# Optimization experiments

Measured on AMD Instinct MI355X. Metric: run time of the kernel, lower is better.

## Reference

```python
import jax, jax.numpy as jnp
import numpy as np

T = 16384       # video length (frames)
C = 7           # out_features = d_model = num surgical phases
F_DIM = 2048    # mstcn_f_dim (spatial feature dim)
LEN_Q = 30      # sliding window length
N_HEADS = 4
D_K = 64        # attn_dim = min(64, mstcn_f_maps=64)
D_FF = 64       # d_ff = mstcn_f_maps


def setup_inputs() -> dict:
    key = jax.random.key(0)
    ks = jax.random.split(key, 10)
    w = lambda i, shape: jax.random.normal(ks[i], shape, jnp.float32) * 0.05
    return {
        "x": jax.random.normal(ks[0], (1, C, T), jnp.float32),
        "long_feature": jax.random.normal(ks[1], (1, T, F_DIM), jnp.float32),
        "W_fc": w(2, (C, F_DIM)),              # nn.Linear(mstcn_f_dim, out_features, bias=False)
        "W_q": w(3, (N_HEADS * D_K, C)),
        "W_k": w(4, (N_HEADS * D_K, C)),
        "W_v": w(5, (N_HEADS * D_K, C)),
        "W_o": w(6, (C, N_HEADS * D_K)),
        "ln1_g": jnp.ones((C,), jnp.float32),
        "ln1_b": jnp.zeros((C,), jnp.float32),
        "W_ff1": w(7, (D_FF, C)),
        "W_ff2": w(8, (C, D_FF)),
        "ln2_g": jnp.ones((C,), jnp.float32),
        "ln2_b": jnp.zeros((C,), jnp.float32),
    }


def layer_norm(x, g, b, eps=1e-5):
    mu = x.mean(-1, keepdims=True)
    var = ((x - mu) ** 2).mean(-1, keepdims=True)
    return (x - mu) * jax.lax.rsqrt(var + eps) * g + b


def reference(x, long_feature, W_fc, W_q, W_k, W_v, W_o, ln1_g, ln1_b, W_ff1, W_ff2, ln2_g, ln2_b):
    # --- vectorized sliding-window (replaces the Python loop of zeros/cat/stack) ---
    feats = x[0].T                                            # (T, C)
    padded = jnp.concatenate([jnp.zeros((LEN_Q - 1, C), feats.dtype), feats], axis=0)
    idx = jnp.arange(T)[:, None] + jnp.arange(LEN_Q)[None, :]  # window ends at frame i
    inputs = padded[idx]                                       # (T, LEN_Q, C)

    # --- spatial embedding: feas = tanh(fc(long_feature)).transpose(0,1) ---
    feas = jnp.tanh(long_feature[0] @ W_fc.T)[:, None, :]      # (T, 1, C)

    # --- decoder layer: cross MHA(query=feas, kv=inputs) + residual + LN ---
    q = (feas @ W_q.T).reshape(T, 1, N_HEADS, D_K).transpose(0, 2, 1, 3)       # (T,H,1,Dk)
    k = (inputs @ W_k.T).reshape(T, LEN_Q, N_HEADS, D_K).transpose(0, 2, 1, 3)  # (T,H,Lq,Dk)
    v = (inputs @ W_v.T).reshape(T, LEN_Q, N_HEADS, D_K).transpose(0, 2, 1, 3)  # (T,H,Lq,Dk)
    scores = jnp.einsum('thqd,thkd->thqk', q, k) / np.float32(np.sqrt(D_K))
    attn = jax.nn.softmax(scores, axis=-1)
    ctx = jnp.einsum('thqk,thkd->thqd', attn, v)
    ctx = ctx.transpose(0, 2, 1, 3).reshape(T, 1, N_HEADS * D_K)
    out = layer_norm(ctx @ W_o.T + feas, ln1_g, ln1_b)         # (T, 1, C)

    # --- position-wise FFN + residual + LN ---
    ff = jax.nn.relu(out @ W_ff1.T) @ W_ff2.T
    out = layer_norm(ff + out, ln2_g, ln2_b)
    return out[:, 0]                                           # (T, C) per-frame logits
```

## Files before the change

kernel.cpp:

```cpp
#include <hip/hip_runtime.h>
#include <math.h>

#define T_FRAMES 16384
#define FDIM 2048
#define LQ 30
#define FPB 16

__global__ __launch_bounds__(448) void setup_kernel(
    const float* __restrict__ Wq, const float* __restrict__ Wk,
    const float* __restrict__ Wv, const float* __restrict__ Wo,
    float* __restrict__ AM) {
  const int e = threadIdx.x;
  if (e >= 392) return;
  const int which = e / 196;
  const int r = e % 196;
  const int h = r / 49;
  const int rr = r % 49;
  const int c = rr / 7;
  const int c2 = rr % 7;
  float s = 0.0f;
  if (which == 0) {
    for (int d = 0; d < 64; ++d)
      s = fmaf(Wq[(h * 64 + d) * 7 + c], Wk[(h * 64 + d) * 7 + c2], s);
  } else {
    for (int d = 0; d < 64; ++d)
      s = fmaf(Wo[c * 256 + h * 64 + d], Wv[(h * 64 + d) * 7 + c2], s);
  }
  AM[e] = s;
}

__global__ __launch_bounds__(256) void fused_kernel(
    const float* __restrict__ lf,
    const float* __restrict__ Wfc,
    const float* __restrict__ x,
    const float* __restrict__ AM,
    const float* __restrict__ W1,
    const float* __restrict__ W2,
    const float* __restrict__ ln1g, const float* __restrict__ ln1b,
    const float* __restrict__ ln2g, const float* __restrict__ ln2b,
    float* __restrict__ out) {
  __shared__ float feas_s[FPB][7];
  __shared__ float AM_s[392];
  __shared__ float ft[(FPB + LQ - 1) * 7];
  __shared__ float hpart[FPB][4][7];

  const int tid = threadIdx.x;
  const int lane = tid & 63;
  const int wave = tid >> 6;
  const int t0 = blockIdx.x * FPB;

  for (int i = tid; i < 392; i += 256) AM_s[i] = AM[i];
  for (int i = tid; i < (FPB + LQ - 1) * 7; i += 256) {
    const int row = i / 7, c = i % 7;
    const int s = t0 - (LQ - 1) + row;
    ft[i] = (s >= 0) ? x[c * T_FRAMES + s] : 0.0f;
  }

  const int tf = t0 + wave * 4;
  const float* lfp = lf + (size_t)tf * FDIM;
  float acc[4][7];
#pragma unroll
  for (int fr = 0; fr < 4; ++fr)
#pragma unroll
    for (int c = 0; c < 7; ++c) acc[fr][c] = 0.0f;

  for (int chunk = 0; chunk < 8; ++chunk) {
    const int f = chunk * 256 + lane * 4;
    const float4 a0 = *(const float4*)(lfp + 0 * FDIM + f);
    const float4 a1 = *(const float4*)(lfp + 1 * FDIM + f);
    const float4 a2 = *(const float4*)(lfp + 2 * FDIM + f);
    const float4 a3 = *(const float4*)(lfp + 3 * FDIM + f);
#pragma unroll
    for (int c = 0; c < 7; ++c) {
      const float4 w = *(const float4*)(Wfc + c * FDIM + f);
      acc[0][c] = fmaf(a0.x, w.x, fmaf(a0.y, w.y, fmaf(a0.z, w.z, fmaf(a0.w, w.w, acc[0][c]))));
      acc[1][c] = fmaf(a1.x, w.x, fmaf(a1.y, w.y, fmaf(a1.z, w.z, fmaf(a1.w, w.w, acc[1][c]))));
      acc[2][c] = fmaf(a2.x, w.x, fmaf(a2.y, w.y, fmaf(a2.z, w.z, fmaf(a2.w, w.w, acc[2][c]))));
      acc[3][c] = fmaf(a3.x, w.x, fmaf(a3.y, w.y, fmaf(a3.z, w.z, fmaf(a3.w, w.w, acc[3][c]))));
    }
  }

#pragma unroll
  for (int fr = 0; fr < 4; ++fr) {
#pragma unroll
    for (int c = 0; c < 7; ++c) {
      float v = acc[fr][c];
      for (int off = 32; off > 0; off >>= 1) v += __shfl_down(v, off, 64);
      if (lane == 0) feas_s[wave * 4 + fr][c] = tanhf(v);
    }
  }
  __syncthreads();

  if (tid < FPB * 4) {
    const int f = tid >> 2;
    const int h = tid & 3;
    float fe[7];
#pragma unroll
    for (int c = 0; c < 7; ++c) fe[c] = feas_s[f][c];

    const float* Ah = AM_s + h * 49;
    const float* Mh = AM_s + 196 + h * 49;
    float qk[7];
#pragma unroll
    for (int c2 = 0; c2 < 7; ++c2) {
      float s = 0.0f;
#pragma unroll
      for (int c = 0; c < 7; ++c) s = fmaf(fe[c], Ah[c * 7 + c2], s);
      qk[c2] = s * 0.125f;
    }
    const float* frow = &ft[f * 7];
    float sc[LQ];
    float m = -1e30f;
#pragma unroll
    for (int j = 0; j < LQ; ++j) {
      const float* r = frow + j * 7;
      float s = 0.0f;
#pragma unroll
      for (int c2 = 0; c2 < 7; ++c2) s = fmaf(qk[c2], r[c2], s);
      sc[j] = s;
      m = fmaxf(m, s);
    }
    float sum = 0.0f;
    float wsum[7] = {0, 0, 0, 0, 0, 0, 0};
#pragma unroll
    for (int j = 0; j < LQ; ++j) {
      const float p = __expf(sc[j] - m);
      sum += p;
      const float* r = frow + j * 7;
#pragma unroll
      for (int c2 = 0; c2 < 7; ++c2) wsum[c2] = fmaf(p, r[c2], wsum[c2]);
    }
    const float inv = 1.0f / sum;
#pragma unroll
    for (int c = 0; c < 7; ++c) {
      float s = 0.0f;
#pragma unroll
      for (int c2 = 0; c2 < 7; ++c2) s = fmaf(Mh[c * 7 + c2], wsum[c2], s);
      hpart[f][h][c] = s * inv;
    }
  }
  __syncthreads();

  if (tid < FPB) {
    const int f = tid;
    float v[7];
#pragma unroll
    for (int c = 0; c < 7; ++c)
      v[c] = feas_s[f][c] + hpart[f][0][c] + hpart[f][1][c] + hpart[f][2][c] + hpart[f][3][c];

    float mu = 0.0f;
#pragma unroll
    for (int c = 0; c < 7; ++c) mu += v[c];
    mu *= (1.0f / 7.0f);
    float var = 0.0f;
#pragma unroll
    for (int c = 0; c < 7; ++c) { const float d = v[c] - mu; var = fmaf(d, d, var); }
    var *= (1.0f / 7.0f);
    float rs = rsqrtf(var + 1e-5f);
    float o1[7];
#pragma unroll
    for (int c = 0; c < 7; ++c) o1[c] = (v[c] - mu) * rs * ln1g[c] + ln1b[c];

    float ff[7] = {0, 0, 0, 0, 0, 0, 0};
    for (int k = 0; k < 64; ++k) {
      float hk = 0.0f;
#pragma unroll
      for (int c = 0; c < 7; ++c) hk = fmaf(W1[k * 7 + c], o1[c], hk);
      hk = fmaxf(hk, 0.0f);
#pragma unroll
      for (int c = 0; c < 7; ++c) ff[c] = fmaf(W2[c * 64 + k], hk, ff[c]);
    }

#pragma unroll
    for (int c = 0; c < 7; ++c) v[c] = ff[c] + o1[c];
    mu = 0.0f;
#pragma unroll
    for (int c = 0; c < 7; ++c) mu += v[c];
    mu *= (1.0f / 7.0f);
    var = 0.0f;
#pragma unroll
    for (int c = 0; c < 7; ++c) { const float d = v[c] - mu; var = fmaf(d, d, var); }
    var *= (1.0f / 7.0f);
    rs = rsqrtf(var + 1e-5f);
    const int t = t0 + f;
#pragma unroll
    for (int c = 0; c < 7; ++c)
      out[(size_t)t * 7 + c] = (v[c] - mu) * rs * ln2g[c] + ln2b[c];
  }
}

extern "C" void kernel_launch(void* const* d_in, const int* in_sizes, int n_in,
                              void* d_out, int out_size, void* d_ws, size_t ws_size,
                              hipStream_t stream) {
  const float* x    = (const float*)d_in[0];
  const float* lf   = (const float*)d_in[1];
  const float* Wfc  = (const float*)d_in[2];
  const float* Wq   = (const float*)d_in[3];
  const float* Wk   = (const float*)d_in[4];
  const float* Wv   = (const float*)d_in[5];
  const float* Wo   = (const float*)d_in[6];
  const float* ln1g = (const float*)d_in[7];
  const float* ln1b = (const float*)d_in[8];
  const float* W1   = (const float*)d_in[9];
  const float* W2   = (const float*)d_in[10];
  const float* ln2g = (const float*)d_in[11];
  const float* ln2b = (const float*)d_in[12];
  float* out = (float*)d_out;

  float* AM = (float*)d_ws;

  setup_kernel<<<1, 448, 0, stream>>>(Wq, Wk, Wv, Wo, AM);
  fused_kernel<<<T_FRAMES / FPB, 256, 0, stream>>>(
      lf, Wfc, x, AM, W1, W2, ln1g, ln1b, ln2g, ln2b, out);
}
```

Before: 254.3 us.

## Stage W_fc in LDS, double-buffer feature loads, and process 32 frames per block

Each block now copies the 56 KB W_fc into shared memory and reads weights from LDS instead of global/L2. Each wave handles 8 frames instead of 4, and long_feature loads for the next chunk are prefetched into registers while the current chunk is computed. The aim is to cut redundant weight traffic and hide memory latency on the bandwidth-bound 128 MB feature read. The costs are a 56 KB per-block LDS copy repeated across 512 blocks, lower occupancy from the large LDS footprint and higher register pressure, and fewer blocks overall.

```diff
diff --git a/kernel.cpp b/kernel.cpp
--- a/kernel.cpp
+++ b/kernel.cpp
@@ -4,7 +4,8 @@
 #define T_FRAMES 16384
 #define FDIM 2048
 #define LQ 30
-#define FPB 16
+#define FPB 32
+#define FPW 8
 
 __global__ __launch_bounds__(448) void setup_kernel(
     const float* __restrict__ Wq, const float* __restrict__ Wk,
@@ -39,9 +40,10 @@
     const float* __restrict__ ln1g, const float* __restrict__ ln1b,
     const float* __restrict__ ln2g, const float* __restrict__ ln2b,
     float* __restrict__ out) {
+  __shared__ float wfc_s[7 * FDIM];
+  __shared__ float ft[(FPB + LQ - 1) * 7];
+  __shared__ float AM_s[392];
   __shared__ float feas_s[FPB][7];
-  __shared__ float AM_s[392];
-  __shared__ float ft[(FPB + LQ - 1) * 7];
   __shared__ float hpart[FPB][4][7];
 
   const int tid = threadIdx.x;
@@ -49,44 +51,66 @@
   const int wave = tid >> 6;
   const int t0 = blockIdx.x * FPB;
 
+  {
+    const float4* wsrc = (const float4*)Wfc;
+    float4* wdst = (float4*)wfc_s;
+    for (int i = tid; i < 7 * (FDIM / 4); i += 256) wdst[i] = wsrc[i];
+  }
   for (int i = tid; i < 392; i += 256) AM_s[i] = AM[i];
   for (int i = tid; i < (FPB + LQ - 1) * 7; i += 256) {
     const int row = i / 7, c = i % 7;
     const int s = t0 - (LQ - 1) + row;
     ft[i] = (s >= 0) ? x[c * T_FRAMES + s] : 0.0f;
   }
-
-  const int tf = t0 + wave * 4;
+  __syncthreads();
+
+  const int tf = t0 + wave * FPW;
   const float* lfp = lf + (size_t)tf * FDIM;
-  float acc[4][7];
-#pragma unroll
-  for (int fr = 0; fr < 4; ++fr)
+  const int fl = lane * 4;
+
+  float acc[FPW][7];
+#pragma unroll
+  for (int fr = 0; fr < FPW; ++fr)
 #pragma unroll
     for (int c = 0; c < 7; ++c) acc[fr][c] = 0.0f;
 
+  float4 cur[FPW], nxt[FPW];
+#pragma unroll
+  for (int fr = 0; fr < FPW; ++fr)
+    cur[fr] = *(const float4*)(lfp + (size_t)fr * FDIM + fl);
+
+#pragma unroll
   for (int chunk = 0; chunk < 8; ++chunk) {
-    const int f = chunk * 256 + lane * 4;
-    const float4 a0 = *(const float4*)(lfp + 0 * FDIM + f);
-    const float4 a1 = *(const float4*)(lfp + 1 * FDIM + f);
-    const float4 a2 = *(const float4*)(lfp + 2 * FDIM + f);
-    const float4 a3 = *(const float4*)(lfp + 3 * FDIM + f);
+    if (chunk < 7) {
+      const int fn = (chunk + 1) * 256 + fl;
+#pragma unroll
+      for (int fr = 0; fr < FPW; ++fr)
+        nxt[fr] = *(const float4*)(lfp + (size_t)fr * FDIM + fn);
+    }
+    const int f = chunk * 256 + fl;
 #pragma unroll
     for (int c = 0; c < 7; ++c) {
-      const float4 w = *(const float4*)(Wfc + c * FDIM + f);
-      acc[0][c] = fmaf(a0.x, w.x, fmaf(a0.y, w.y, fmaf(a0.z, w.z, fmaf(a0.w, w.w, acc[0][c]))));
-      acc[1][c] = fmaf(a1.x, w.x, fmaf(a1.y, w.y, fmaf(a1.z, w.z, fmaf(a1.w, w.w, acc[1][c]))));
-      acc[2][c] = fmaf(a2.x, w.x, fmaf(a2.y, w.y, fmaf(a2.z, w.z, fmaf(a2.w, w.w, acc[2][c]))));
-      acc[3][c] = fmaf(a3.x, w.x, fmaf(a3.y, w.y, fmaf(a3.z, w.z, fmaf(a3.w, w.w, acc[3][c]))));
-    }
-  }
-
-#pragma unroll
-  for (int fr = 0; fr < 4; ++fr) {
+      const float4 w = *(const float4*)(&wfc_s[c * FDIM + f]);
+#pragma unroll
+      for (int fr = 0; fr < FPW; ++fr)
+        acc[fr][c] = fmaf(cur[fr].x, w.x,
+                     fmaf(cur[fr].y, w.y,
+                     fmaf(cur[fr].z, w.z,
+                     fmaf(cur[fr].w, w.w, acc[fr][c]))));
+    }
+    if (chunk < 7) {
+#pragma unroll
+      for (int fr = 0; fr < FPW; ++fr) cur[fr] = nxt[fr];
+    }
+  }
+
+#pragma unroll
+  for (int fr = 0; fr < FPW; ++fr) {
 #pragma unroll
     for (int c = 0; c < 7; ++c) {
       float v = acc[fr][c];
       for (int off = 32; off > 0; off >>= 1) v += __shfl_down(v, off, 64);
-      if (lane == 0) feas_s[wave * 4 + fr][c] = tanhf(v);
+      if (lane == 0) feas_s[wave * FPW + fr][c] = tanhf(v);
     }
   }
   __syncthreads();
```

New measurement: 290.8 us. 1.14x slower.
